# Optimization experiments

Measured on AMD Instinct MI355X. Metric: run time of the kernel, lower is better.

The kernel has to match this reference:

```python
import jax, jax.numpy as jnp
import numpy as np

NHEAD, DK, DV, DMODEL, L = 8, 64, 64, 512, 32

def setup_inputs() -> dict:
    key = jax.random.key(0)
    ks = jax.random.split(key, 9)
    B, N = 4, 2048
    s = 1.0 / np.sqrt(DMODEL)
    return {
        "q": jax.random.normal(ks[0], (B, N, DMODEL), jnp.float32),
        "k": jax.random.normal(ks[1], (B, N, DMODEL), jnp.float32),
        "v": jax.random.normal(ks[2], (B, N, DMODEL), jnp.float32),
        "Wq": jax.random.normal(ks[3], (DMODEL, NHEAD * DK), jnp.float32) * s,
        "Wk": jax.random.normal(ks[4], (DMODEL, NHEAD * DK), jnp.float32) * s,
        "Wv": jax.random.normal(ks[5], (DMODEL, NHEAD * DV), jnp.float32) * s,
        "Wfc": jax.random.normal(ks[6], (NHEAD * DV, DMODEL), jnp.float32) * s,
        "ln_g": jnp.ones((DMODEL,), jnp.float32),
        "ln_b": jnp.zeros((DMODEL,), jnp.float32),
    }

def reference(q, k, v, Wq, Wk, Wv, Wfc, ln_g, ln_b):
    B, Nq, _ = q.shape
    residual = q
    # project and split heads: [B, H, N, d]
    qh = (q @ Wq).reshape(B, Nq, NHEAD, DK).transpose(0, 2, 1, 3)
    kh = (k @ Wk).reshape(B, k.shape[1], NHEAD, DK).transpose(0, 2, 1, 3)
    vh = (v @ Wv).reshape(B, v.shape[1], NHEAD, DV).transpose(0, 2, 1, 3)
    # scaled dot-product scores and softmax over keys
    attn = jnp.einsum('bhqd,bhkd->bhqk', qh / jnp.sqrt(jnp.float32(DK)), kh)
    attn = jax.nn.softmax(attn, axis=-1)
    # AWG: keep entries >= l-th largest per row, renormalize
    threshold = jax.lax.top_k(attn, L)[0][..., -1:]  # [B,H,Nq,1]
    W = jnp.where(attn >= threshold, attn, 0.0)
    W_out = W / jnp.sum(W, axis=-1, keepdims=True)
    out = jnp.einsum('bhqk,bhkd->bhqd', W_out, vh)
    out = out.transpose(0, 2, 1, 3).reshape(B, Nq, NHEAD * DV)
    out = out @ Wfc + residual
    # LayerNorm, eps=1e-6
    mu = jnp.mean(out, axis=-1, keepdims=True)
    var = jnp.var(out, axis=-1, keepdims=True)
    return (out - mu) / jnp.sqrt(var + 1e-6) * ln_g + ln_b
```

## Files before the change

### kernel.cpp

```cpp
#include <hip/hip_runtime.h>
#include <hip/hip_fp16.h>

#define BATCH 4
#define NSEQ 2048
#define DMODEL 512
#define NHEAD 8
#define HDIM 64
#define LSEL 32
#define MAXL 64
#define QROWS 16
#define CSTRIDE 331

typedef __attribute__((ext_vector_type(8))) _Float16 f16x8;
typedef __attribute__((ext_vector_type(4))) float f32x4;
typedef unsigned long long ull;

__device__ inline ushort f2h(float x) { __half h = __float2half(x); return *reinterpret_cast<ushort*>(&h); }
__device__ inline float h16f(ushort u) { __half t; *reinterpret_cast<ushort*>(&t) = u; return __half2float(t); }
__device__ inline float sort2f(uint su) {
    ushort hb = (su & 0x8000u) ? (ushort)(su ^ 0x8000u) : (ushort)(su ^ 0xFFFFu);
    return h16f(hb);
}
__device__ inline uint sm2(uint w) {
    uint s = (w >> 15) & 0x00010001u;
    uint m = s * 0x7FFFu;
    return w ^ (m | 0x80008000u);
}

__global__ __launch_bounds__(256) void cvtA_kernel(
    const float* __restrict__ q, const float* __restrict__ k, const float* __restrict__ v,
    ushort* __restrict__ q16, ushort* __restrict__ k16, ushort* __restrict__ v16)
{
    const int z = blockIdx.y;
    const float* src = (z == 0) ? q : (z == 1) ? k : v;
    ushort* dst = (z == 0) ? q16 : (z == 1) ? k16 : v16;
    const size_t base = (size_t)blockIdx.x * 2048 + threadIdx.x * 4;
    float4 fa = *(const float4*)(src + base);
    float4 fb = *(const float4*)(src + base + 1024);
    ushort4 ha = {f2h(fa.x), f2h(fa.y), f2h(fa.z), f2h(fa.w)};
    ushort4 hb = {f2h(fb.x), f2h(fb.y), f2h(fb.z), f2h(fb.w)};
    *(ushort4*)(dst + base) = ha;
    *(ushort4*)(dst + base + 1024) = hb;
}

__global__ __launch_bounds__(256) void cvtW_kernel(
    const float* __restrict__ Wq, const float* __restrict__ Wk,
    const float* __restrict__ Wv, const float* __restrict__ Wfc,
    ushort* __restrict__ Wt)
{
    const int z = blockIdx.y;
    const float* W = (z == 0) ? Wq : (z == 1) ? Wk : (z == 2) ? Wv : Wfc;
    ushort* O = Wt + (size_t)z * DMODEL * DMODEL;
    const int gt = blockIdx.x * 256 + threadIdx.x;
    const int n = gt & 511;
    const int kc = (gt >> 9) * 16;
    uint pk[8];
#pragma unroll
    for (int i = 0; i < 8; ++i) {
        uint lo = f2h(W[(size_t)(kc + 2 * i) * DMODEL + n]);
        uint hi = f2h(W[(size_t)(kc + 2 * i + 1) * DMODEL + n]);
        pk[i] = lo | (hi << 16);
    }
    uint4 u0 = {pk[0], pk[1], pk[2], pk[3]};
    uint4 u1 = {pk[4], pk[5], pk[6], pk[7]};
    *(uint4*)(O + (size_t)n * DMODEL + kc) = u0;
    *(uint4*)(O + (size_t)n * DMODEL + kc + 8) = u1;
}

template<int MODE>
__global__ __launch_bounds__(256, 2) void hgemm_kernel(
    const ushort* __restrict__ A0, const ushort* __restrict__ A1, const ushort* __restrict__ A2,
    const ushort* __restrict__ Wt,
    ushort* __restrict__ O0, ushort* __restrict__ O1, ushort* __restrict__ O2,
    float* __restrict__ Ofc)
{
    __shared__ ushort Ah[64][40];
    __shared__ ushort Bh[512][40];

    const int tid = threadIdx.x;
    const int wave = tid >> 6, lane = tid & 63;
    const int lr = lane & 15, lg = lane >> 4;
    const int bm = blockIdx.x * 64;
    const int z = blockIdx.y;

    const ushort* A16 = (MODE == 0) ? (z == 0 ? A0 : z == 1 ? A1 : A2) : A0;
    const ushort* Wz = Wt + (size_t)((MODE == 0) ? z : 3) * (DMODEL * DMODEL);

    f32x4 acc[4][8];
#pragma unroll
    for (int i = 0; i < 4; ++i)
#pragma unroll
        for (int j = 0; j < 8; ++j) acc[i][j] = (f32x4){0.f, 0.f, 0.f, 0.f};

    const int sar = tid >> 2, sak = (tid & 3) * 8;

    for (int k0 = 0; k0 < DMODEL; k0 += 32) {
        __syncthreads();
        *(uint4*)&Ah[sar][sak] = *(const uint4*)(A16 + (size_t)(bm + sar) * DMODEL + k0 + sak);
#pragma unroll
        for (int i = 0; i < 8; ++i) {
            int n = sar + 64 * i;
            *(uint4*)&Bh[n][sak] = *(const uint4*)(Wz + (size_t)n * DMODEL + k0 + sak);
        }
        __syncthreads();
        f16x8 af[4];
#pragma unroll
        for (int fr = 0; fr < 4; ++fr) af[fr] = *(const f16x8*)&Ah[fr * 16 + lr][lg * 8];
#pragma unroll
        for (int fc2 = 0; fc2 < 8; ++fc2) {
            f16x8 bf = *(const f16x8*)&Bh[wave * 128 + fc2 * 16 + lr][lg * 8];
#pragma unroll
            for (int fr = 0; fr < 4; ++fr)
                acc[fr][fc2] = __builtin_amdgcn_mfma_f32_16x16x32_f16(af[fr], bf, acc[fr][fc2], 0, 0, 0);
        }
    }

    if (MODE == 1) {
#pragma unroll
        for (int fr = 0; fr < 4; ++fr)
#pragma unroll
            for (int fc2 = 0; fc2 < 8; ++fc2)
#pragma unroll
                for (int r = 0; r < 4; ++r)
                    Ofc[(size_t)(bm + fr * 16 + lg * 4 + r) * DMODEL + wave * 128 + fc2 * 16 + lr] = acc[fr][fc2][r];
        return;
    }

    const float osc = (z == 0) ? 0.125f : 1.0f;
    ushort* O = (z == 0) ? O0 : (z == 1) ? O1 : O2;
    const int b = bm >> 11;
    const int nseq0 = bm & (NSEQ - 1);
    ushort* smw = (ushort*)&Bh[0][0] + wave * (64 * 72);
#pragma unroll
    for (int hp = 0; hp < 2; ++hp) {
        __syncthreads();
#pragma unroll
        for (int f4 = 0; f4 < 4; ++f4) {
            int fc2 = hp * 4 + f4;
            int nl = f4 * 16 + lr;
#pragma unroll
            for (int fr = 0; fr < 4; ++fr)
#pragma unroll
                for (int r = 0; r < 4; ++r)
                    smw[(fr * 16 + lg * 4 + r) * 72 + nl] = f2h(acc[fr][fc2][r] * osc);
        }
        __syncthreads();
        const int h = wave * 2 + hp;
        ushort* obase = O + ((size_t)(b * NHEAD + h) * NSEQ + nseq0) * HDIM;
#pragma unroll
        for (int i = 0; i < 8; ++i) {
            int m = i * 8 + (lane >> 3);
            int dc = (lane & 7) * 8;
            *(uint4*)(obase + (size_t)m * HDIM + dc) = *(const uint4*)(smw + m * 72 + dc);
        }
    }
}

__device__ inline int wave_sum6(int c) {
    int tot = (int)__popcll(__ballot(c & 1));
    tot += (int)__popcll(__ballot(c & 2)) << 1;
    tot += (int)__popcll(__ballot(c & 4)) << 2;
    tot += (int)__popcll(__ballot(c & 8)) << 3;
    tot += (int)__popcll(__ballot(c & 16)) << 4;
    tot += (int)__popcll(__ballot(c & 32)) << 5;
    return tot;
}

__device__ uint full_thr(const ushort* Sr, int lane, uint lo0) {
    uint flo = lo0, fhi = 0xFFFFu;
#pragma unroll 1
    for (int it2 = 0; it2 < 16; ++it2) {
        uint mid = (flo + fhi + 1) >> 1, M = mid << 16;
        int cl = 0;
#pragma unroll
        for (int it = 0; it < 4; ++it) {
            uint4 r4 = *(const uint4*)(Sr + it * 512 + lane * 8);
            cl += ((r4.x << 16) >= M) + ((r4.x & 0xFFFF0000u) >= M);
            cl += ((r4.y << 16) >= M) + ((r4.y & 0xFFFF0000u) >= M);
            cl += ((r4.z << 16) >= M) + ((r4.z & 0xFFFF0000u) >= M);
            cl += ((r4.w << 16) >= M) + ((r4.w & 0xFFFF0000u) >= M);
        }
        bool ge = wave_sum6(cl) >= LSEL;
        flo = ge ? mid : flo;
        fhi = ge ? fhi : mid - 1;
    }
    return flo;
}

__device__ int recount(const ushort* Sr, int lane, uint th) {
    int cs = 0;
#pragma unroll
    for (int it = 0; it < 4; ++it) {
        uint4 r4 = *(const uint4*)(Sr + it * 512 + lane * 8);
        cs += ((r4.x << 16) >= th) + ((r4.x & 0xFFFF0000u) >= th);
        cs += ((r4.y << 16) >= th) + ((r4.y & 0xFFFF0000u) >= th);
        cs += ((r4.z << 16) >= th) + ((r4.z & 0xFFFF0000u) >= th);
        cs += ((r4.w << 16) >= th) + ((r4.w & 0xFFFF0000u) >= th);
    }
    return cs;
}

__device__ float extract_big(const ushort* Sr, int lane, uint th, float Mv,
                             int pre, uint* selrow)
{
    const float L2E = 1.4426950408889634f;
    float wp = 0.f;
    int pos = pre;
#pragma unroll
    for (int it = 0; it < 4; ++it) {
        uint4 r4 = *(const uint4*)(Sr + it * 512 + lane * 8);
        uint ib = (uint)(it * 512 + lane * 8);
        uint wds[4] = {r4.x, r4.y, r4.z, r4.w};
#pragma unroll
        for (int c = 0; c < 4; ++c) {
            uint vL = wds[c] << 16, vH = wds[c] & 0xFFFF0000u;
            if (vL >= th) {
                ushort w16 = f2h(exp2f((sort2f(vL >> 16) - Mv) * L2E));
                if (pos < MAXL) { selrow[pos] = ((uint)w16 << 16) | (ib + c * 2); wp += h16f(w16); }
                ++pos;
            }
            if (vH >= th) {
                ushort w16 = f2h(exp2f((sort2f(vH >> 16) - Mv) * L2E));
                if (pos < MAXL) { selrow[pos] = ((uint)w16 << 16) | (ib + c * 2 + 1); wp += h16f(w16); }
                ++pos;
            }
        }
    }
#pragma unroll
    for (int off = 32; off >= 1; off >>= 1) wp += __shfl_xor(wp, off);
    return wp;
}

#define INS5(T0, T1, T2, T3, T4, P) { \
    uint m1_ = min(P, T0); T0 = max(P, T0); \
    uint m2_ = min(m1_, T1); T1 = max(m1_, T1); \
    uint m3_ = min(m2_, T2); T2 = max(m2_, T2); \
    uint m4_ = min(m3_, T3); T3 = max(m3_, T3); \
    T4 = max(m4_, T4); }

__global__ __launch_bounds__(512, 8) void attn_kernel(
    const ushort* __restrict__ qh, const ushort* __restrict__ kh,
    const ushort* __restrict__ vh, ushort* __restrict__ ao)
{
    __shared__ uint cand[QROWS * CSTRIDE];
    __shared__ __align__(16) uint sel[QROWS][MAXL];
    __shared__ __align__(16) ushort Sb1[2056];
    __shared__ float wsums[QROWS];
    __shared__ int   nks[QROWS];
    __shared__ int   missflag[QROWS];

    const int tid = threadIdx.x;
    const int wave = tid >> 6;
    const int lane = tid & 63;
    const int bh = blockIdx.y;
    const int q0 = blockIdx.x * QROWS;
    const int lr = lane & 15;
    const int lg = lane >> 4;
    const float L2E = 1.4426950408889634f;

    const ushort* Qb = qh + ((size_t)bh * NSEQ + q0) * HDIM;
    const ushort* Kb = kh + (size_t)bh * NSEQ * HDIM;

    f16x8 qf0 = *(const f16x8*)(Qb + lr * HDIM + lg * 8);
    f16x8 qf1 = *(const f16x8*)(Qb + lr * HDIM + 32 + lg * 8);

    uint sA0 = 0, sA1 = 0, sA2 = 0, sA3 = 0, sA4 = 0;
    uint sB0 = 0, sB1 = 0, sB2 = 0, sB3 = 0, sB4 = 0;

    const int kwbase = wave * 256;
    const ushort* Kt0 = Kb + (size_t)kwbase * HDIM;
    f16x8 a0 = *(const f16x8*)(Kt0 + lr * HDIM + lg * 8);
    f16x8 a1 = *(const f16x8*)(Kt0 + lr * HDIM + 32 + lg * 8);

#pragma unroll
    for (int t = 0; t < 16; ++t) {
        f16x8 n0 = a0, n1 = a1;
        if (t < 15) {
            const ushort* Kn = Kb + (size_t)(kwbase + (t + 1) * 16) * HDIM;
            n0 = *(const f16x8*)(Kn + lr * HDIM + lg * 8);
            n1 = *(const f16x8*)(Kn + lr * HDIM + 32 + lg * 8);
        }
        f32x4 acc = {0.f, 0.f, 0.f, 0.f};
        acc = __builtin_amdgcn_mfma_f32_16x16x32_f16(a0, qf0, acc, 0, 0, 0);
        acc = __builtin_amdgcn_mfma_f32_16x16x32_f16(a1, qf1, acc, 0, 0, 0);
        const uint col = (uint)(kwbase + t * 16 + lg * 4);
        uint w0 = (uint)f2h(acc[0]) | ((uint)f2h(acc[1]) << 16);
        uint w1 = (uint)f2h(acc[2]) | ((uint)f2h(acc[3]) << 16);
        w0 = sm2(w0); w1 = sm2(w1);
        uint p;
        p = (w0 << 16) | col;               INS5(sA0, sA1, sA2, sA3, sA4, p);
        p = (w0 & 0xFFFF0000u) | (col + 1); INS5(sA0, sA1, sA2, sA3, sA4, p);
        p = (w1 << 16) | (col + 2);         INS5(sB0, sB1, sB2, sB3, sB4, p);
        p = (w1 & 0xFFFF0000u) | (col + 3); INS5(sB0, sB1, sB2, sB3, sB4, p);
        a0 = n0; a1 = n1;
    }

    {
        const int sid = wave * 8 + lg * 2;
        const int cb = lr * CSTRIDE + sid;
        cand[cb +   0] = sA0; cand[cb +  66] = sA1; cand[cb + 132] = sA2;
        cand[cb + 198] = sA3; cand[cb + 264] = sA4;
        cand[cb +   1] = sB0; cand[cb +  67] = sB1; cand[cb + 133] = sB2;
        cand[cb + 199] = sB3; cand[cb + 265] = sB4;
    }
    __syncthreads();

    const int halfid = lane >> 5;
    const int s = lane & 31;
    const int qr = wave * 2 + halfid;
    const int b = bh >> 3, hh = bh & 7;
    const ull LOMASK = 0xFFFFFFFFull;
    const ull HB = halfid ? ~LOMASK : LOMASK;

    uint c0, c1, c2, c3, c4, c5, c6, c7, c8, c9;
    {
        const int cb = qr * CSTRIDE + s;
        c0 = cand[cb];       c1 = cand[cb +  66]; c2 = cand[cb + 132];
        c3 = cand[cb + 198]; c4 = cand[cb + 264];
        c5 = cand[cb + 32];       c6 = cand[cb +  66 + 32]; c7 = cand[cb + 132 + 32];
        c8 = cand[cb + 198 + 32]; c9 = cand[cb + 264 + 32];
    }

    uint mx = max(c0, c5);
#pragma unroll
    for (int off = 1; off <= 16; off <<= 1) mx = max(mx, (uint)__shfl_xor((int)mx, off));
    const float Mv = sort2f(mx >> 16);

    uint lo = 0, hi = 0xFFFFu;
#pragma unroll
    for (int it = 0; it < 16; ++it) {
        uint mid = (lo + hi + 1) >> 1, M = mid << 16;
        int cnt = (c0 >= M) + (c1 >= M) + (c2 >= M) + (c3 >= M) + (c4 >= M)
                + (c5 >= M) + (c6 >= M) + (c7 >= M) + (c8 >= M) + (c9 >= M);
        ull m0 = __ballot(cnt & 1), m1 = __ballot(cnt & 2);
        ull m2 = __ballot(cnt & 4), m3 = __ballot(cnt & 8);
        int tH = (int)__popcll(m0 & HB) + 2 * (int)__popcll(m1 & HB)
               + 4 * (int)__popcll(m2 & HB) + 8 * (int)__popcll(m3 & HB);
        bool ge = tH >= LSEL;
        lo = ge ? mid : lo;
        hi = ge ? hi : mid - 1;
    }
    const uint th = lo << 16;

    ull mm = __ballot((c4 >= th) || (c9 >= th));
    const bool missMy = (mm & HB) != 0ull;

    if (!missMy) {
        int csel = (c0 >= th) + (c1 >= th) + (c2 >= th) + (c3 >= th)
                 + (c5 >= th) + (c6 >= th) + (c7 >= th) + (c8 >= th);
        ull below = ((1ull << lane) - 1ull) & HB;
        int pre = 0, tot = 0;
#pragma unroll
        for (int bb = 0; bb < 4; ++bb) {
            ull m = __ballot((csel >> bb) & 1);
            pre += (int)__popcll(m & below) << bb;
            tot += (int)__popcll(m & HB) << bb;
        }
        uint regs[8] = {c0, c1, c2, c3, c5, c6, c7, c8};
        float wp = 0.f;
        int k2 = 0;
#pragma unroll
        for (int i = 0; i < 8; ++i) {
            uint ui = regs[i];
            if (ui >= th) {
                ushort w16 = f2h(exp2f((sort2f(ui >> 16) - Mv) * L2E));
                int pos = pre + k2;
                if (pos < MAXL) { sel[qr][pos] = ((uint)w16 << 16) | (ui & 0xFFFFu); wp += h16f(w16); }
                ++k2;
            }
        }
#pragma unroll
        for (int off = 1; off <= 16; off <<= 1) wp += __shfl_xor(wp, off);
        if (s == 0) { wsums[qr] = wp; nks[qr] = (tot < MAXL) ? tot : MAXL; }
    }
    if (s == 0) missflag[qr] = missMy ? 1 : 0;
    __syncthreads();

    for (int r = 0; r < QROWS; ++r) {
        if (missflag[r]) {
            __syncthreads();
#pragma unroll 4
            for (int t = 0; t < 16; ++t) {
                const ushort* Kt = Kb + (size_t)(kwbase + t * 16) * HDIM;
                f16x8 ra0 = *(const f16x8*)(Kt + lr * HDIM + lg * 8);
                f16x8 ra1 = *(const f16x8*)(Kt + lr * HDIM + 32 + lg * 8);
                f32x4 ac2 = {0.f, 0.f, 0.f, 0.f};
                ac2 = __builtin_amdgcn_mfma_f32_16x16x32_f16(ra0, qf0, ac2, 0, 0, 0);
                ac2 = __builtin_amdgcn_mfma_f32_16x16x32_f16(ra1, qf1, ac2, 0, 0, 0);
                if (lr == r) {
                    uint w0 = (uint)f2h(ac2[0]) | ((uint)f2h(ac2[1]) << 16);
                    uint w1 = (uint)f2h(ac2[2]) | ((uint)f2h(ac2[3]) << 16);
                    uint2 pk = {sm2(w0), sm2(w1)};
                    *(uint2*)&Sb1[kwbase + t * 16 + lg * 4] = pk;
                }
            }
            __syncthreads();
            if (wave == (r >> 1)) {
                const int h = r & 1;
                const float Mvr = __shfl(Mv, h * 32);
                const uint lor = (uint)__shfl((int)lo, h * 32);
                uint ft = full_thr(Sb1, lane, lor);
                uint thv = ft << 16;
                int cs = recount(Sb1, lane, thv);
                ull below64 = (1ull << lane) - 1ull;
                int preS = 0, totS = 0;
#pragma unroll
                for (int bb = 0; bb < 6; ++bb) {
                    ull m = __ballot((cs >> bb) & 1);
                    preS += (int)__popcll(m & below64) << bb;
                    totS += (int)__popcll(m) << bb;
                }
                float wr = extract_big(Sb1, lane, thv, Mvr, preS, &sel[r][0]);
                if (lane == 0) { wsums[r] = wr; nks[r] = (totS < MAXL) ? totS : MAXL; }
            }
        }
    }
    __syncthreads();

    const __half2* V2 = reinterpret_cast<const __half2*>(vh + (size_t)bh * NSEQ * HDIM);
    const int dp = lane & 31;
    const int nkMy = nks[qr];
    const float wsMy = wsums[qr];
    const uint* selp = &sel[qr][0];

    float ox = 0.f, oy = 0.f;
    int j = 0;
    for (; j + 8 <= nkMy; j += 8) {
        uint e[8];
        *(uint4*)&e[0] = *(const uint4*)(selp + j);
        *(uint4*)&e[4] = *(const uint4*)(selp + j + 4);
        float2 vv[8];
        float ww[8];
#pragma unroll
        for (int i2 = 0; i2 < 8; ++i2) {
            int idx = (int)(e[i2] & 0xFFFFu);
            ww[i2] = h16f((ushort)(e[i2] >> 16));
            vv[i2] = __half22float2(V2[(size_t)idx * 32 + dp]);
        }
#pragma unroll
        for (int i2 = 0; i2 < 8; ++i2) { ox += ww[i2] * vv[i2].x; oy += ww[i2] * vv[i2].y; }
    }
    for (; j < nkMy; ++j) {
        uint e = selp[j];
        int idx = (int)(e & 0xFFFFu);
        float w = h16f((ushort)(e >> 16));
        float2 v0 = __half22float2(V2[(size_t)idx * 32 + dp]);
        ox += w * v0.x; oy += w * v0.y;
    }

    const float inv = 1.f / wsMy;
    uint opk = (uint)f2h(ox * inv) | ((uint)f2h(oy * inv) << 16);
    *(uint*)(ao + ((size_t)(b * NSEQ) + q0 + qr) * DMODEL + hh * HDIM + dp * 2) = opk;
}

__global__ __launch_bounds__(256) void ln_kernel(
    const float* __restrict__ fcr, const float* __restrict__ resid,
    const float* __restrict__ g, const float* __restrict__ bta, float* __restrict__ out)
{
    const int row = blockIdx.x * 4 + (threadIdx.x >> 6);
    const int lane = threadIdx.x & 63;
    const size_t base = (size_t)row * DMODEL + lane * 8;
    float4 xa = *(const float4*)(fcr + base);
    float4 xb = *(const float4*)(fcr + base + 4);
    float4 ra = *(const float4*)(resid + base);
    float4 rb = *(const float4*)(resid + base + 4);
    xa.x += ra.x; xa.y += ra.y; xa.z += ra.z; xa.w += ra.w;
    xb.x += rb.x; xb.y += rb.y; xb.z += rb.z; xb.w += rb.w;
    float sum = xa.x + xa.y + xa.z + xa.w + xb.x + xb.y + xb.z + xb.w;
    float sq = xa.x * xa.x + xa.y * xa.y + xa.z * xa.z + xa.w * xa.w
             + xb.x * xb.x + xb.y * xb.y + xb.z * xb.z + xb.w * xb.w;
#pragma unroll
    for (int off = 32; off >= 1; off >>= 1) {
        sum += __shfl_xor(sum, off);
        sq += __shfl_xor(sq, off);
    }
    float mean = sum * (1.f / 512.f);
    float var = sq * (1.f / 512.f) - mean * mean;
    float rstd = rsqrtf(var + 1e-6f);
    float4 ga = *(const float4*)(g + lane * 8);
    float4 gb = *(const float4*)(g + lane * 8 + 4);
    float4 ba = *(const float4*)(bta + lane * 8);
    float4 bb = *(const float4*)(bta + lane * 8 + 4);
    float4 oa, ob;
    oa.x = (xa.x - mean) * rstd * ga.x + ba.x;
    oa.y = (xa.y - mean) * rstd * ga.y + ba.y;
    oa.z = (xa.z - mean) * rstd * ga.z + ba.z;
    oa.w = (xa.w - mean) * rstd * ga.w + ba.w;
    ob.x = (xb.x - mean) * rstd * gb.x + bb.x;
    ob.y = (xb.y - mean) * rstd * gb.y + bb.y;
    ob.z = (xb.z - mean) * rstd * gb.z + bb.z;
    ob.w = (xb.w - mean) * rstd * gb.w + bb.w;
    *(float4*)(out + base) = oa;
    *(float4*)(out + base + 4) = ob;
}

extern "C" void kernel_launch(void* const* d_in, const int* in_sizes, int n_in,
                              void* d_out, int out_size, void* d_ws, size_t ws_size,
                              hipStream_t stream)
{
    (void)in_sizes; (void)n_in; (void)out_size; (void)ws_size;

    const float* q   = (const float*)d_in[0];
    const float* k   = (const float*)d_in[1];
    const float* v   = (const float*)d_in[2];
    const float* Wq  = (const float*)d_in[3];
    const float* Wk  = (const float*)d_in[4];
    const float* Wv  = (const float*)d_in[5];
    const float* Wfc = (const float*)d_in[6];
    const float* g   = (const float*)d_in[7];
    const float* b   = (const float*)d_in[8];
    float* out = (float*)d_out;

    const size_t SZ = (size_t)BATCH * NSEQ * DMODEL;
    const size_t WSZ = (size_t)DMODEL * DMODEL;
    ushort* w16 = (ushort*)d_ws;
    ushort* q16 = w16;
    ushort* k16 = w16 + SZ;
    ushort* v16 = w16 + 2 * SZ;
    ushort* Wt  = w16 + 3 * SZ;
    ushort* qh  = Wt + 4 * WSZ;
    ushort* kh  = qh + SZ;
    ushort* vh  = kh + SZ;
    ushort* ao  = vh + SZ;
    float* fc_raw = (float*)d_ws;

    cvtA_kernel<<<dim3(2048, 3), 256, 0, stream>>>(q, k, v, q16, k16, v16);
    cvtW_kernel<<<dim3(64, 4), 256, 0, stream>>>(Wq, Wk, Wv, Wfc, Wt);
    hgemm_kernel<0><<<dim3(128, 3), 256, 0, stream>>>(q16, k16, v16, Wt, qh, kh, vh, nullptr);
    attn_kernel<<<dim3(NSEQ / QROWS, BATCH * NHEAD), 512, 0, stream>>>(qh, kh, vh, ao);
    hgemm_kernel<1><<<dim3(128, 1), 256, 0, stream>>>(ao, nullptr, nullptr, Wt, nullptr, nullptr, nullptr, fc_raw);
    ln_kernel<<<(BATCH * NSEQ) / 4, 256, 0, stream>>>(fc_raw, q, g, b, out);
}
```

Before: 325.7 us.

## Stage K tiles through swizzled LDS with coalesced loads and XCD-aware block remap

The first score pass now loads K through a shared-memory tile. The whole block does contiguous 16-byte global loads, writes them into an XOR-swizzled Ktile buffer, and each wave then reads its 16-key fragments from LDS, so the key order per wave becomes interleaved. Block indices are remapped so that consecutive blocks for the same batch-head land on the same XCD, which should improve L2 reuse of K. Launch bounds drop to 4 blocks per SM to make room for the extra 16KB of LDS. The cost is two __syncthreads per iteration, an unroll-1 loop and lower occupancy. The top-k and fallback logic are unchanged.

```diff
diff --git a/kernel.cpp b/kernel.cpp
--- a/kernel.cpp
+++ b/kernel.cpp
@@ -23,9 +23,10 @@
 }
 __device__ inline uint sm2(uint w) {
     uint s = (w >> 15) & 0x00010001u;
-    uint m = s * 0x7FFFu;
+    uint m = (s << 15) - s;
     return w ^ (m | 0x80008000u);
 }
+__device__ inline uint swzb(uint b) { return b ^ (((b >> 7) & 7u) << 4); }
 
 __global__ __launch_bounds__(256) void cvtA_kernel(
     const float* __restrict__ q, const float* __restrict__ k, const float* __restrict__ v,
@@ -238,10 +239,11 @@
     uint m4_ = min(m3_, T3); T3 = max(m3_, T3); \
     T4 = max(m4_, T4); }
 
-__global__ __launch_bounds__(512, 8) void attn_kernel(
+__global__ __launch_bounds__(512, 4) void attn_kernel(
     const ushort* __restrict__ qh, const ushort* __restrict__ kh,
     const ushort* __restrict__ vh, ushort* __restrict__ ao)
 {
+    __shared__ __align__(16) ushort Ktile[8192];
     __shared__ uint cand[QROWS * CSTRIDE];
     __shared__ __align__(16) uint sel[QROWS][MAXL];
     __shared__ __align__(16) ushort Sb1[2056];
@@ -252,8 +254,13 @@
     const int tid = threadIdx.x;
     const int wave = tid >> 6;
     const int lane = tid & 63;
-    const int bh = blockIdx.y;
-    const int q0 = blockIdx.x * QROWS;
+
+    const int wid = blockIdx.y * gridDim.x + blockIdx.x;
+    const int cpx = (gridDim.x * gridDim.y) >> 3;
+    const int flat = (wid & 7) * cpx + (wid >> 3);
+    const int bh = flat >> 7;
+    const int q0 = (flat & 127) * QROWS;
+
     const int lr = lane & 15;
     const int lg = lane >> 4;
     const float L2E = 1.4426950408889634f;
@@ -267,23 +274,35 @@
     uint sA0 = 0, sA1 = 0, sA2 = 0, sA3 = 0, sA4 = 0;
     uint sB0 = 0, sB1 = 0, sB2 = 0, sB3 = 0, sB4 = 0;
 
-    const int kwbase = wave * 256;
-    const ushort* Kt0 = Kb + (size_t)kwbase * HDIM;
-    f16x8 a0 = *(const f16x8*)(Kt0 + lr * HDIM + lg * 8);
-    f16x8 a1 = *(const f16x8*)(Kt0 + lr * HDIM + 32 + lg * 8);
-
-#pragma unroll
+    uint4 r0, r1;
+    {
+        const ushort* src = Kb + tid * 16;
+        r0 = *(const uint4*)(src);
+        r1 = *(const uint4*)(src + 8);
+    }
+    const uint wb0 = swzb((uint)tid * 32) >> 1;
+    const uint wb1 = swzb((uint)tid * 32 + 16) >> 1;
+    const uint klocal = (uint)(wave * 16 + lr);
+    const uint rb0 = swzb(klocal * 128 + lg * 16) >> 1;
+    const uint rb1 = swzb(klocal * 128 + 64 + lg * 16) >> 1;
+
+#pragma unroll 1
     for (int t = 0; t < 16; ++t) {
-        f16x8 n0 = a0, n1 = a1;
+        __syncthreads();
+        *(uint4*)&Ktile[wb0] = r0;
+        *(uint4*)&Ktile[wb1] = r1;
+        __syncthreads();
         if (t < 15) {
-            const ushort* Kn = Kb + (size_t)(kwbase + (t + 1) * 16) * HDIM;
-            n0 = *(const f16x8*)(Kn + lr * HDIM + lg * 8);
-            n1 = *(const f16x8*)(Kn + lr * HDIM + 32 + lg * 8);
-        }
+            const ushort* src = Kb + (t + 1) * 8192 + tid * 16;
+            r0 = *(const uint4*)(src);
+            r1 = *(const uint4*)(src + 8);
+        }
+        f16x8 a0 = *(const f16x8*)&Ktile[rb0];
+        f16x8 a1 = *(const f16x8*)&Ktile[rb1];
         f32x4 acc = {0.f, 0.f, 0.f, 0.f};
         acc = __builtin_amdgcn_mfma_f32_16x16x32_f16(a0, qf0, acc, 0, 0, 0);
         acc = __builtin_amdgcn_mfma_f32_16x16x32_f16(a1, qf1, acc, 0, 0, 0);
-        const uint col = (uint)(kwbase + t * 16 + lg * 4);
+        const uint col = (uint)(t * 128 + wave * 16 + lg * 4);
         uint w0 = (uint)f2h(acc[0]) | ((uint)f2h(acc[1]) << 16);
         uint w1 = (uint)f2h(acc[2]) | ((uint)f2h(acc[3]) << 16);
         w0 = sm2(w0); w1 = sm2(w1);
@@ -292,7 +311,6 @@
         p = (w0 & 0xFFFF0000u) | (col + 1); INS5(sA0, sA1, sA2, sA3, sA4, p);
         p = (w1 << 16) | (col + 2);         INS5(sB0, sB1, sB2, sB3, sB4, p);
         p = (w1 & 0xFFFF0000u) | (col + 3); INS5(sB0, sB1, sB2, sB3, sB4, p);
-        a0 = n0; a1 = n1;
     }
 
     {
@@ -376,6 +394,7 @@
     if (s == 0) missflag[qr] = missMy ? 1 : 0;
     __syncthreads();
 
+    const int kwbase = wave * 256;
     for (int r = 0; r < QROWS; ++r) {
         if (missflag[r]) {
             __syncthreads();
```

New measurement: 320.9 us. No clear change (-1.5%).
